# Kernel optimization log

Measured on AMD Instinct MI355X. Metric: run time of the kernel, lower is better.

The kernel has to match this reference:

```python
import jax, jax.numpy as jnp
import numpy as np

N_NODES = 50000
N_EDGES = 800000
IN_DIM = 128
HIDDEN = 128


def setup_inputs() -> dict:
    key = jax.random.key(0)
    ks = jax.random.split(key, 8)
    feat = jax.random.normal(ks[0], (N_NODES, IN_DIM), dtype=jnp.float32)
    hx = jax.random.normal(ks[1], (N_NODES, HIDDEN), dtype=jnp.float32)
    src = jax.random.randint(ks[2], (N_EDGES,), 0, N_NODES, dtype=jnp.int32)
    dst = jax.random.randint(ks[3], (N_EDGES,), 0, N_NODES, dtype=jnp.int32)
    s_i = 1.0 / np.sqrt(IN_DIM)
    s_h = 1.0 / np.sqrt(HIDDEN)
    W_i = jax.random.uniform(ks[4], (IN_DIM, 3 * HIDDEN), jnp.float32, -s_i, s_i)
    b_i = jnp.zeros((3 * HIDDEN,), jnp.float32)
    W_h = jax.random.uniform(ks[5], (HIDDEN, 3 * HIDDEN), jnp.float32, -s_h, s_h)
    b_h = jnp.zeros((3 * HIDDEN,), jnp.float32)
    return {"feat": feat, "hx": hx, "W_i": W_i, "b_i": b_i,
            "W_h": W_h, "b_h": b_h, "src": src, "dst": dst}


def _graph_conv(x, W, b, src, dst, norm_src, norm_dst):
    # DGL GraphConv, norm='both', in_feats < out_feats path:
    # scale by out-degree^{-1/2} of src, aggregate-sum to dst,
    # scale by in-degree^{-1/2} of dst, then linear.
    x = x * norm_src[:, None]                      # [N, d]
    agg = jax.ops.segment_sum(x[src], dst, num_segments=N_NODES)  # [N, d]
    agg = agg * norm_dst[:, None]
    return agg @ W + b                             # [N, 3*hidden]


def reference(feat, hx, W_i, b_i, W_h, b_h, src, dst):
    ones = jnp.ones((src.shape[0],), jnp.float32)
    deg_out = jax.ops.segment_sum(ones, src, num_segments=N_NODES)
    deg_in = jax.ops.segment_sum(ones, dst, num_segments=N_NODES)
    norm_src = jax.lax.rsqrt(jnp.clip(deg_out, 1.0))
    norm_dst = jax.lax.rsqrt(jnp.clip(deg_in, 1.0))

    i = _graph_conv(feat, W_i, b_i, src, dst, norm_src, norm_dst)
    h = _graph_conv(hx, W_h, b_h, src, dst, norm_src, norm_dst)

    i_r, i_z, i_n = jnp.split(i, 3, axis=-1)
    h_r, h_z, h_n = jnp.split(h, 3, axis=-1)
    r = jax.nn.sigmoid(i_r + h_r)
    z = jax.nn.sigmoid(i_z + h_z)
    n = jnp.tanh(i_n + r * h_n)
    return (1.0 - z) * n + z * hx
```

## Files before the change

kernel.cpp:

```cpp
#include <hip/hip_runtime.h>
#include <math.h>

#define DIM 128
#define NCH 32
#define NMAXW 25024

typedef float f32x4v __attribute__((ext_vector_type(4)));
typedef short bf16x8 __attribute__((ext_vector_type(8)));

static __device__ __forceinline__ short f2bf(float f) {
    unsigned u = __float_as_uint(f);
    unsigned r = (u + 0x7fffu + ((u >> 16) & 1u)) >> 16;
    return (short)r;
}
static __device__ __forceinline__ float bf2f(unsigned short s) {
    return __uint_as_float(((unsigned)s) << 16);
}

__global__ __launch_bounds__(1024) void k_hist(const int* __restrict__ src,
                                               const int* __restrict__ dst,
                                               unsigned short* __restrict__ partO,
                                               unsigned short* __restrict__ partI,
                                               unsigned short* __restrict__ rank,
                                               int N, int Npad, int E, int chunk) {
    __shared__ unsigned int h[NMAXW];
    int t = threadIdx.x;
    int isI = blockIdx.x < NCH;
    int c = isI ? blockIdx.x : blockIdx.x - NCH;
    int NW = (N + 1) >> 1;
    for (int i = t; i < NW; i += 1024) h[i] = 0;
    __syncthreads();
    int e0 = c * chunk, e1 = min(e0 + chunk, E);
    if (isI) {
        for (int e = e0 + t; e < e1; e += 1024) {
            int d = dst[e];
            unsigned sh = (d & 1) * 16;
            unsigned old = atomicAdd(&h[d >> 1], 1u << sh);
            rank[e] = (unsigned short)((old >> sh) & 0xffffu);
        }
    } else {
        for (int e = e0 + t; e < e1; e += 1024) {
            int s = src[e];
            atomicAdd(&h[s >> 1], 1u << ((s & 1) * 16));
        }
    }
    __syncthreads();
    unsigned int* p = (unsigned int*)((isI ? partI : partO) + (size_t)c * Npad);
    for (int i = t; i < NW; i += 1024) p[i] = h[i];
}

__global__ __launch_bounds__(256) void k_bsum(const unsigned short* __restrict__ partI,
                                              int* __restrict__ bsum, int N, int Npad) {
    __shared__ int red[4];
    int b = blockIdx.x, t = threadIdx.x;
    int n = b * 256 + t;
    int s = 0;
    if (n < N) {
        #pragma unroll
        for (int c = 0; c < NCH; ++c) s += partI[(size_t)c * Npad + n];
    }
    for (int off = 32; off; off >>= 1) s += __shfl_down(s, off);
    if ((t & 63) == 0) red[t >> 6] = s;
    __syncthreads();
    if (t == 0) bsum[b] = red[0] + red[1] + red[2] + red[3];
}

__global__ __launch_bounds__(256) void k_off(const unsigned short* __restrict__ partI,
                                             const unsigned short* __restrict__ partO,
                                             const int* __restrict__ bsum,
                                             int* __restrict__ csrOffC,
                                             int* __restrict__ csrOff,
                                             float* __restrict__ normIf,
                                             float* __restrict__ normOf,
                                             int N, int Npad, int NB) {
    __shared__ int sp[256];
    __shared__ int sbase;
    int b = blockIdx.x, t = threadIdx.x;
    int own = (t < NB) ? bsum[t] : 0;
    sp[t] = own;
    __syncthreads();
    for (int off = 1; off < 256; off <<= 1) {
        int u = (t >= off) ? sp[t - off] : 0;
        __syncthreads();
        sp[t] += u;
        __syncthreads();
    }
    if (t == b) sbase = sp[t] - own;
    if (b == 0 && t == NB - 1) csrOff[N] = sp[t];
    __syncthreads();
    int n = b * 256 + t;
    int cv[NCH];
    int tI = 0, tO = 0;
    if (n < N) {
        #pragma unroll
        for (int c = 0; c < NCH; ++c) {
            cv[c] = partI[(size_t)c * Npad + n];
            tI += cv[c];
            tO += partO[(size_t)c * Npad + n];
        }
    }
    sp[t] = tI;
    __syncthreads();
    for (int off = 1; off < 256; off <<= 1) {
        int u = (t >= off) ? sp[t - off] : 0;
        __syncthreads();
        sp[t] += u;
        __syncthreads();
    }
    int o = sbase + sp[t] - tI;
    if (n < N) {
        csrOff[n] = o;
        normIf[n] = rsqrtf(fmaxf((float)tI, 1.0f));
        normOf[n] = rsqrtf(fmaxf((float)tO, 1.0f));
        int base = o;
        #pragma unroll
        for (int c = 0; c < NCH; ++c) {
            csrOffC[(size_t)c * N + n] = base;
            base += cv[c];
        }
    }
}

__global__ __launch_bounds__(256) void k_xcw(const float* __restrict__ feat,
                                             const float* __restrict__ hx,
                                             const float* __restrict__ Wi,
                                             const float* __restrict__ Wh,
                                             const float* __restrict__ normOf,
                                             short* __restrict__ Wbf,
                                             short* __restrict__ fh, int N) {
    int i = blockIdx.x * 256 + threadIdx.x;
    int T1 = N * 64;
    if (i < T1) {
        int n = i >> 6, q = i & 63;
        float ns = normOf[n];
        const float* spp = (q < 32) ? &feat[(size_t)n * 128 + q * 4]
                                    : &hx[(size_t)n * 128 + (q - 32) * 4];
        float4 v = *(const float4*)spp;
        short4 p;
        p.x = f2bf(v.x * ns); p.y = f2bf(v.y * ns);
        p.z = f2bf(v.z * ns); p.w = f2bf(v.w * ns);
        *(short4*)&fh[(size_t)n * 256 + q * 4] = p;
    } else {
        int w = i - T1;
        if (w < 98304) {
            int k = w & 127, n = (w >> 7) & 15, r = w >> 11;
            int gm = r % 6, cb = r / 6;
            const float* Wsrc = (gm < 3) ? Wi : Wh;
            int g = gm % 3;
            Wbf[w] = f2bf(Wsrc[k * 384 + g * 128 + cb * 16 + n]);
        }
    }
}

__global__ __launch_bounds__(256) void k_fill(const int* __restrict__ src,
                                              const int* __restrict__ dst,
                                              const unsigned short* __restrict__ rank,
                                              const int* __restrict__ csrOffC,
                                              int* __restrict__ srcSorted,
                                              int N, int E, int chunk) {
    int e = blockIdx.x * 256 + threadIdx.x;
    if (e < E) {
        int c = e / chunk;
        int pos = csrOffC[(size_t)c * N + dst[e]] + (int)rank[e];
        srcSorted[pos] = src[e];
    }
}

__global__ __launch_bounds__(256) void gather_kernel(
    const short* __restrict__ fh, const int* __restrict__ csrOff,
    const int* __restrict__ srcSorted, const float* __restrict__ normIf,
    short* __restrict__ agg, int N) {
    int wv = threadIdx.x >> 6, lane = threadIdx.x & 63;
    int d = blockIdx.x * 4 + wv;
    if (d >= N) return;
    const ushort4* fh4 = (const ushort4*)fh;
    int beg = csrOff[d], end = csrOff[d + 1];
    float4 acc = make_float4(0.f, 0.f, 0.f, 0.f);
    #pragma unroll 8
    for (int e = beg; e < end; ++e) {
        int s = srcSorted[e];
        ushort4 v = fh4[(size_t)s * 64 + lane];
        acc.x += bf2f(v.x); acc.y += bf2f(v.y);
        acc.z += bf2f(v.z); acc.w += bf2f(v.w);
    }
    float nd = normIf[d];
    short4 p;
    p.x = f2bf(acc.x * nd); p.y = f2bf(acc.y * nd);
    p.z = f2bf(acc.z * nd); p.w = f2bf(acc.w * nd);
    *(short4*)&agg[(size_t)d * 256 + lane * 4] = p;
}

#define GLOAD_LDS16(gp, lp)                                                   \
    __builtin_amdgcn_global_load_lds(                                         \
        (const __attribute__((address_space(1))) void*)(gp),                  \
        (__attribute__((address_space(3))) void*)(lp), 16, 0, 0)

__global__ __launch_bounds__(256, 3) void gemm_gates_kernel(
    const short* __restrict__ agg, const float* __restrict__ hx,
    const short* __restrict__ Wbf,
    const float* __restrict__ bi, const float* __restrict__ bh,
    float* __restrict__ out, int N) {
    __shared__ short wlds[2][12288];
    const int tid = threadIdx.x;
    const int wv = tid >> 6, lane = tid & 63;
    const int l15 = lane & 15, quad = lane >> 4;
    const int rowBase = (blockIdx.x * 4 + wv) * 16;
    const bool active = rowBase < N;

    int arow = active ? rowBase + l15 : 0;
    const short* aPtr = agg + (size_t)arow * 256;
    bf16x8 aLo[4], aHi[4];
    #pragma unroll
    for (int kst = 0; kst < 4; ++kst) {
        aLo[kst] = *(const bf16x8*)&aPtr[kst * 32 + quad * 8];
        aHi[kst] = *(const bf16x8*)&aPtr[128 + kst * 32 + quad * 8];
    }

    {
        const char* gs = (const char*)Wbf;
        #pragma unroll
        for (int i = 0; i < 6; ++i) {
            int ldsByte = wv * 6144 + i * 1024 + lane * 16;
            int gByte = ldsByte ^ (((ldsByte >> 8) & 15) << 4);
            GLOAD_LDS16(gs + gByte, (char*)&wlds[0][0] + wv * 6144 + i * 1024);
        }
    }
    __syncthreads();

    for (int cb = 0; cb < 8; ++cb) {
        const int buf = cb & 1;
        if (cb < 7) {
            const char* gs = (const char*)(Wbf + (size_t)(cb + 1) * 12288);
            #pragma unroll
            for (int i = 0; i < 6; ++i) {
                int ldsByte = wv * 6144 + i * 1024 + lane * 16;
                int gByte = ldsByte ^ (((ldsByte >> 8) & 15) << 4);
                GLOAD_LDS16(gs + gByte,
                            (char*)&wlds[buf ^ 1][0] + wv * 6144 + i * 1024);
            }
        }
        if (active) {
            int ocol = cb * 16 + l15;
            float hv[4];
            #pragma unroll
            for (int reg = 0; reg < 4; ++reg)
                hv[reg] = hx[(size_t)(rowBase + quad * 4 + reg) * DIM + ocol];
            float bir = bi[ocol], biz = bi[128 + ocol], bin = bi[256 + ocol];
            float bhr = bh[ocol], bhz = bh[128 + ocol], bhn = bh[256 + ocol];

            f32x4v acc[6];
            #pragma unroll
            for (int g = 0; g < 6; ++g) acc[g] = (f32x4v){0.f, 0.f, 0.f, 0.f};
            const char* slab = (const char*)&wlds[buf][0];
            #pragma unroll
            for (int kst = 0; kst < 4; ++kst) {
                const int co = (((kst * 4 + quad) ^ l15) << 4);
                #pragma unroll
                for (int g = 0; g < 3; ++g) {
                    bf16x8 bI = *(const bf16x8*)(slab + g * 4096 + l15 * 256 + co);
                    acc[g] = __builtin_amdgcn_mfma_f32_16x16x32_bf16(
                        aLo[kst], bI, acc[g], 0, 0, 0);
                    bf16x8 bH = *(const bf16x8*)(slab + (g + 3) * 4096 + l15 * 256 + co);
                    acc[g + 3] = __builtin_amdgcn_mfma_f32_16x16x32_bf16(
                        aHi[kst], bH, acc[g + 3], 0, 0, 0);
                }
            }
            #pragma unroll
            for (int reg = 0; reg < 4; ++reg) {
                int row = rowBase + quad * 4 + reg;
                float ir = acc[0][reg] + bir, iz = acc[1][reg] + biz, in_ = acc[2][reg] + bin;
                float hr = acc[3][reg] + bhr, hz = acc[4][reg] + bhz, hn = acc[5][reg] + bhn;
                float rg = 1.0f / (1.0f + __expf(-(ir + hr)));
                float zg = 1.0f / (1.0f + __expf(-(iz + hz)));
                float ng = tanhf(in_ + rg * hn);
                out[(size_t)row * DIM + ocol] = (1.0f - zg) * ng + zg * hv[reg];
            }
        }
        __syncthreads();
    }
}

extern "C" void kernel_launch(void* const* d_in, const int* in_sizes, int n_in,
                              void* d_out, int out_size, void* d_ws, size_t ws_size,
                              hipStream_t stream) {
    const float* feat = (const float*)d_in[0];
    const float* hx   = (const float*)d_in[1];
    const float* Wi   = (const float*)d_in[2];
    const float* bi   = (const float*)d_in[3];
    const float* Wh   = (const float*)d_in[4];
    const float* bh   = (const float*)d_in[5];
    const int* src    = (const int*)d_in[6];
    const int* dst    = (const int*)d_in[7];
    float* out        = (float*)d_out;

    int N = in_sizes[0] / DIM;
    int E = in_sizes[6];
    int Npad = (N + 1) & ~1;
    int chunk = (E + NCH - 1) / NCH;
    int NB    = (N + 255) / 256;

    unsigned short* partI = (unsigned short*)d_ws;
    unsigned short* partO = partI + (size_t)NCH * Npad;
    int* csrOffC   = (int*)(partO + (size_t)NCH * Npad);
    int* csrOff    = csrOffC + (size_t)NCH * N;
    int* srcSorted = csrOff + N + 1;
    unsigned short* rank = (unsigned short*)(srcSorted + E);
    int* bsum      = (int*)(rank + ((E + 1) & ~1));
    float* normIf  = (float*)(bsum + 256);
    float* normOf  = normIf + N;
    size_t iend = (size_t)(normOf + N - (float*)d_ws);
    size_t wofs = (iend * 4 + 15) & ~(size_t)15;
    short* Wbf = (short*)((char*)d_ws + wofs);
    size_t fofs = (wofs + 98304 * 2 + 15) & ~(size_t)15;
    short* fh = (short*)((char*)d_ws + fofs);
    short* agg = (short*)d_out;

    k_hist<<<2 * NCH, 1024, 0, stream>>>(src, dst, partO, partI, rank,
                                         N, Npad, E, chunk);
    k_bsum<<<NB, 256, 0, stream>>>(partI, bsum, N, Npad);
    k_off<<<NB, 256, 0, stream>>>(partI, partO, bsum, csrOffC, csrOff,
                                  normIf, normOf, N, Npad, NB);
    k_xcw<<<(N * 64 + 98304 + 255) / 256, 256, 0, stream>>>(
        feat, hx, Wi, Wh, normOf, Wbf, fh, N);
    k_fill<<<(E + 255) / 256, 256, 0, stream>>>(
        src, dst, rank, csrOffC, srcSorted, N, E, chunk);

    gather_kernel<<<(N + 3) / 4, 256, 0, stream>>>(
        fh, csrOff, srcSorted, normIf, agg, N);
    gemm_gates_kernel<<<(N + 63) / 64, 256, 0, stream>>>(
        agg, hx, Wbf, bi, bh, out, N);
}
```

Baseline: 246.1 us.

## Fuse preprocessing kernels to cut launches: bsum into hist, W convert, fill into xcw

Folds the per-block in-degree sum into the histogram kernel, which now reduces its shared-memory histogram and adds into bsum with atomics after a memset. The weight-to-bf16 conversion moves into extra blocks of the histogram kernel, and the CSR fill is merged into the feature-scaling kernel. This drops two kernel launches and the separate pass over partI, at the cost of an extra memset and global atomics on bsum. The hist kernel's 96 weight-conversion blocks share a launch with the 64 heavy histogram blocks.

```diff
diff --git a/kernel.cpp b/kernel.cpp
--- a/kernel.cpp
+++ b/kernel.cpp
@@ -19,10 +19,25 @@
 
 __global__ __launch_bounds__(1024) void k_hist(const int* __restrict__ src,
                                                const int* __restrict__ dst,
+                                               const float* __restrict__ Wi,
+                                               const float* __restrict__ Wh,
                                                unsigned short* __restrict__ partO,
                                                unsigned short* __restrict__ partI,
                                                unsigned short* __restrict__ rank,
+                                               short* __restrict__ Wbf,
+                                               int* __restrict__ bsum,
                                                int N, int Npad, int E, int chunk) {
+    if (blockIdx.x >= 2 * NCH) {
+        int w = (blockIdx.x - 2 * NCH) * 1024 + threadIdx.x;
+        if (w < 98304) {
+            int k = w & 127, n = (w >> 7) & 15, r = w >> 11;
+            int gm = r % 6, cb = r / 6;
+            const float* Wsrc = (gm < 3) ? Wi : Wh;
+            int g = gm % 3;
+            Wbf[w] = f2bf(Wsrc[k * 384 + g * 128 + cb * 16 + n]);
+        }
+        return;
+    }
     __shared__ unsigned int h[NMAXW];
     int t = threadIdx.x;
     int isI = blockIdx.x < NCH;
@@ -47,22 +62,24 @@
     __syncthreads();
     unsigned int* p = (unsigned int*)((isI ? partI : partO) + (size_t)c * Npad);
     for (int i = t; i < NW; i += 1024) p[i] = h[i];
-}
-
-__global__ __launch_bounds__(256) void k_bsum(const unsigned short* __restrict__ partI,
-                                              int* __restrict__ bsum, int N, int Npad) {
-    __shared__ int red[4];
-    int b = blockIdx.x, t = threadIdx.x;
-    int n = b * 256 + t;
-    int s = 0;
-    if (n < N) {
-        #pragma unroll
-        for (int c = 0; c < NCH; ++c) s += partI[(size_t)c * Npad + n];
-    }
-    for (int off = 32; off; off >>= 1) s += __shfl_down(s, off);
-    if ((t & 63) == 0) red[t >> 6] = s;
-    __syncthreads();
-    if (t == 0) bsum[b] = red[0] + red[1] + red[2] + red[3];
+    if (isI) {
+        int NBp = (N + 255) >> 8;
+        for (int g = t >> 6; g < NBp; g += 16) {
+            int lane = t & 63;
+            int n0 = g * 256;
+            int s = 0;
+            #pragma unroll
+            for (int j = 0; j < 2; ++j) {
+                int wi = (n0 >> 1) + lane + j * 64;
+                if (wi < NW && wi < ((n0 + 256 + 1) >> 1)) {
+                    unsigned v = h[wi];
+                    s += (int)(v & 0xffffu) + (int)(v >> 16);
+                }
+            }
+            for (int off = 32; off; off >>= 1) s += __shfl_down(s, off);
+            if (lane == 0 && s) atomicAdd(&bsum[g], s);
+        }
+    }
 }
 
 __global__ __launch_bounds__(256) void k_off(const unsigned short* __restrict__ partI,
@@ -123,11 +140,14 @@
 
 __global__ __launch_bounds__(256) void k_xcw(const float* __restrict__ feat,
                                              const float* __restrict__ hx,
-                                             const float* __restrict__ Wi,
-                                             const float* __restrict__ Wh,
                                              const float* __restrict__ normOf,
-                                             short* __restrict__ Wbf,
-                                             short* __restrict__ fh, int N) {
+                                             short* __restrict__ fh,
+                                             const int* __restrict__ src,
+                                             const int* __restrict__ dst,
+                                             const unsigned short* __restrict__ rank,
+                                             const int* __restrict__ csrOffC,
+                                             int* __restrict__ srcSorted,
+                                             int N, int E, int chunk) {
     int i = blockIdx.x * 256 + threadIdx.x;
     int T1 = N * 64;
     if (i < T1) {
@@ -141,28 +161,12 @@
         p.z = f2bf(v.z * ns); p.w = f2bf(v.w * ns);
         *(short4*)&fh[(size_t)n * 256 + q * 4] = p;
     } else {
-        int w = i - T1;
-        if (w < 98304) {
-            int k = w & 127, n = (w >> 7) & 15, r = w >> 11;
-            int gm = r % 6, cb = r / 6;
-            const float* Wsrc = (gm < 3) ? Wi : Wh;
-            int g = gm % 3;
-            Wbf[w] = f2bf(Wsrc[k * 384 + g * 128 + cb * 16 + n]);
-        }
-    }
-}
-
-__global__ __launch_bounds__(256) void k_fill(const int* __restrict__ src,
-                                              const int* __restrict__ dst,
-                                              const unsigned short* __restrict__ rank,
-                                              const int* __restrict__ csrOffC,
-                                              int* __restrict__ srcSorted,
-                                              int N, int E, int chunk) {
-    int e = blockIdx.x * 256 + threadIdx.x;
-    if (e < E) {
-        int c = e / chunk;
-        int pos = csrOffC[(size_t)c * N + dst[e]] + (int)rank[e];
-        srcSorted[pos] = src[e];
+        int e = i - T1;
+        if (e < E) {
+            int c = e / chunk;
+            int pos = csrOffC[(size_t)c * N + dst[e]] + (int)rank[e];
+            srcSorted[pos] = src[e];
+        }
     }
 }
 
@@ -315,15 +319,14 @@
     short* fh = (short*)((char*)d_ws + fofs);
     short* agg = (short*)d_out;
 
-    k_hist<<<2 * NCH, 1024, 0, stream>>>(src, dst, partO, partI, rank,
-                                         N, Npad, E, chunk);
-    k_bsum<<<NB, 256, 0, stream>>>(partI, bsum, N, Npad);
+    hipMemsetAsync(bsum, 0, 256 * sizeof(int), stream);
+    k_hist<<<2 * NCH + 96, 1024, 0, stream>>>(src, dst, Wi, Wh,
+                                              partO, partI, rank, Wbf, bsum,
+                                              N, Npad, E, chunk);
     k_off<<<NB, 256, 0, stream>>>(partI, partO, bsum, csrOffC, csrOff,
                                   normIf, normOf, N, Npad, NB);
-    k_xcw<<<(N * 64 + 98304 + 255) / 256, 256, 0, stream>>>(
-        feat, hx, Wi, Wh, normOf, Wbf, fh, N);
-    k_fill<<<(E + 255) / 256, 256, 0, stream>>>(
-        src, dst, rank, csrOffC, srcSorted, N, E, chunk);
+    k_xcw<<<(N * 64 + E + 255) / 256, 256, 0, stream>>>(
+        feat, hx, normOf, fh, src, dst, rank, csrOffC, srcSorted, N, E, chunk);
 
     gather_kernel<<<(N + 3) / 4, 256, 0, stream>>>(
         fh, csrOff, srcSorted, normIf, agg, N);
```

Measured after the change: 259.6 us. +5.5%, slower.
